# Optimization experiments

Hardware: AMD Instinct MI355X
Metric: run time of the kernel (lower is better)

Reference implementation:

```python
import jax, jax.numpy as jnp
import numpy as np

ROUTINGS = 3
NUM_CAPSULE = 32
DIM_CAPSULE = 64


def squash(x, axis=-1):
    # scale = sqrt(||x||^2 + eps) / (0.5 + ||x||^2 + eps)
    sq = jnp.sum(x * x, axis=axis, keepdims=True) + 1e-7
    return (jnp.sqrt(sq) / (0.5 + sq)) * x


def setup_inputs() -> dict:
    key = jax.random.key(0)
    k1, k2 = jax.random.split(key)
    B, IN, ID = 64, 1024, 256
    u_vecs = jax.random.normal(k1, (B, IN, ID), dtype=jnp.float32)
    # nn.Linear weight [NC*DC, ID], xavier_normal init
    fan_out, fan_in = NUM_CAPSULE * DIM_CAPSULE, ID
    std = np.sqrt(2.0 / (fan_in + fan_out)).astype(np.float32)
    W = jax.random.normal(k2, (fan_out, fan_in), dtype=jnp.float32) * std
    return {"u_vecs": u_vecs, "W": W}


def reference(u_vecs, W):
    B, IN, ID = u_vecs.shape
    # Linear projection: [B, IN, NC*DC]
    u_hat = jnp.einsum('bid,od->bio', u_vecs, W)
    # -> [B, NC, IN, DC]
    u_hat = u_hat.reshape(B, IN, NUM_CAPSULE, DIM_CAPSULE).transpose(0, 2, 1, 3)

    b = jnp.zeros((B, NUM_CAPSULE, IN), dtype=u_hat.dtype)
    o = None
    for i in range(ROUTINGS):
        c = jax.nn.softmax(b, axis=1)                      # softmax over output capsules
        o = jnp.einsum('bni,bnid->bnd', c, u_hat)          # [B, NC, DC]
        if i < ROUTINGS - 1:
            # F.normalize(o, 2, -1): x / max(||x||, 1e-12)
            norm = jnp.linalg.norm(o, axis=-1, keepdims=True)
            o = o / jnp.maximum(norm, 1e-12)
            b = jnp.einsum('bnid,bnd->bni', u_hat, o)
    return squash(o)
```

## Files before the change

kernel.cpp:

```cpp
#include <hip/hip_runtime.h>
#include <math.h>


#define B   64
#define IN  1024
#define ID  256
#define NC  32
#define DC  64

__global__ __launch_bounds__(256) void k_sumu(const float* __restrict__ u,
                                              float* __restrict__ sp0) {
    const int c = blockIdx.x, b = blockIdx.y;
    const int d = threadIdx.x;
    const float* up = u + ((size_t)b * IN + (size_t)c * (IN / 8)) * ID + d;
    float acc = 0.f;
#pragma unroll 8
    for (int i = 0; i < IN / 8; ++i) acc += up[(size_t)i * ID];
    sp0[(c * B + b) * ID + d] = acc;
}

__global__ __launch_bounds__(256) void k_ot(const float* __restrict__ W,
                                            const float* __restrict__ src,
                                            float* __restrict__ tout,
                                            const int mode) {
    const int bn = blockIdx.x;
    const int b = bn / NC, n = bn % NC;
    __shared__ float s_lds[ID];
    __shared__ float o_lds[DC];
    __shared__ float on_lds[DC];
    const int tid = threadIdx.x;

    float sv = 0.f;
    if (mode == 0) {
#pragma unroll
        for (int c = 0; c < 8; ++c) sv += src[(c * B + b) * ID + tid];
        sv *= (1.0f / NC);
    } else {
#pragma unroll
        for (int c = 0; c < 8; ++c) sv += src[((size_t)(c * B + b) * NC + n) * ID + tid];
    }
    s_lds[tid] = sv;
    __syncthreads();

    const int wave = tid >> 6, lane = tid & 63;
    const float* Wn = W + (size_t)n * DC * ID;
#pragma unroll 4
    for (int r = 0; r < 16; ++r) {
        const int d = wave * 16 + r;
        const float* wrow = Wn + (size_t)d * ID;
        float p = wrow[lane]        * s_lds[lane]
                + wrow[lane + 64]   * s_lds[lane + 64]
                + wrow[lane + 128]  * s_lds[lane + 128]
                + wrow[lane + 192]  * s_lds[lane + 192];
#pragma unroll
        for (int off = 32; off > 0; off >>= 1) p += __shfl_down(p, off);
        if (lane == 0) o_lds[d] = p;
    }
    __syncthreads();

    if (mode == 2) {
        if (tid < DC) {
            float v = o_lds[tid];
            float sq = v * v;
#pragma unroll
            for (int off = 32; off > 0; off >>= 1) sq += __shfl_down(sq, off);
            sq = __shfl(sq, 0) + 1e-7f;
            const float sc = sqrtf(sq) / (0.5f + sq);
            tout[(size_t)(b * NC + n) * DC + tid] = v * sc;
        }
        return;
    }

    if (tid < DC) {
        float v = o_lds[tid];
        float sq = v * v;
#pragma unroll
        for (int off = 32; off > 0; off >>= 1) sq += __shfl_down(sq, off);
        sq = __shfl(sq, 0);
        const float inv = 1.0f / fmaxf(sqrtf(sq), 1e-12f);
        on_lds[tid] = v * inv;
    }
    __syncthreads();

    float acc = 0.f;
    const float* wc = Wn + tid;
#pragma unroll 8
    for (int d = 0; d < DC; ++d) acc += wc[(size_t)d * ID] * on_lds[d];
    tout[((size_t)b * NC + n) * ID + tid] = acc;
}

#define ITILE 128
__global__ __launch_bounds__(256) void k_bl(const float* __restrict__ u,
                                            const float* __restrict__ t,
                                            float* __restrict__ bl) {
    const int it = blockIdx.x, b = blockIdx.y;
    const int iBase = it * ITILE;
    __shared__ float Ts[ID][36];
    __shared__ float Us[16][132];
    const int tid = threadIdx.x;

    {
        const float* tb = t + (size_t)b * NC * ID;
#pragma unroll
        for (int n = 0; n < NC; ++n) Ts[tid][n] = tb[(size_t)n * ID + tid];
    }

    const int q = tid >> 3;
    const int r = tid & 7;
    float acc[4][4] = {{0.f}};
    const float* ub = u + ((size_t)b * IN + iBase) * ID;

    for (int kc = 0; kc < ID / 16; ++kc) {
        __syncthreads();
#pragma unroll
        for (int rep = 0; rep < 2; ++rep) {
            const int f = tid + rep * 256;
            const int i = f >> 2, c4 = f & 3;
            const float4 v = *(const float4*)(ub + (size_t)i * ID + kc * 16 + c4 * 4);
            Us[c4 * 4 + 0][i] = v.x;
            Us[c4 * 4 + 1][i] = v.y;
            Us[c4 * 4 + 2][i] = v.z;
            Us[c4 * 4 + 3][i] = v.w;
        }
        __syncthreads();
#pragma unroll
        for (int k = 0; k < 16; ++k) {
            const float4 a4 = *(const float4*)&Us[k][q * 4];
            const float4 b4 = *(const float4*)&Ts[kc * 16 + k][r * 4];
            const float av[4] = {a4.x, a4.y, a4.z, a4.w};
            const float bv[4] = {b4.x, b4.y, b4.z, b4.w};
#pragma unroll
            for (int ii = 0; ii < 4; ++ii)
#pragma unroll
                for (int jj = 0; jj < 4; ++jj) acc[ii][jj] += av[ii] * bv[jj];
        }
    }

    float* blb = bl + ((size_t)b * IN + iBase) * NC;
#pragma unroll
    for (int ii = 0; ii < 4; ++ii) {
        const float4 v = make_float4(acc[ii][0], acc[ii][1], acc[ii][2], acc[ii][3]);
        *(float4*)&blb[(size_t)(q * 4 + ii) * NC + r * 4] = v;
    }
}

#define AITILE 128
__global__ __launch_bounds__(256) void k_agg(const float* __restrict__ u,
                                             const float* __restrict__ bl,
                                             float* __restrict__ sp) {
    const int c = blockIdx.x, b = blockIdx.y;
    const int iBase = c * AITILE;
    __shared__ float c_lds[AITILE][36];
    const int tid = threadIdx.x;

    {
        const int i = tid >> 1, half = tid & 1;
        const float* blp = bl + ((size_t)b * IN + iBase + i) * NC + half * 16;
        float v[16];
#pragma unroll
        for (int j = 0; j < 16; ++j) v[j] = blp[j];
        float mx = v[0];
#pragma unroll
        for (int j = 1; j < 16; ++j) mx = fmaxf(mx, v[j]);
        mx = fmaxf(mx, __shfl_xor(mx, 1));
        float sum = 0.f;
#pragma unroll
        for (int j = 0; j < 16; ++j) { v[j] = __expf(v[j] - mx); sum += v[j]; }
        sum += __shfl_xor(sum, 1);
        const float inv = 1.0f / sum;
#pragma unroll
        for (int j = 0; j < 16; ++j) c_lds[i][half * 16 + j] = v[j] * inv;
    }
    __syncthreads();

    const int d4 = tid & 63;
    const int ng = tid >> 6;
    float acc[8][4] = {{0.f}};
    const float* ub = u + ((size_t)b * IN + iBase) * ID + d4 * 4;
    for (int i = 0; i < AITILE; ++i) {
        const float4 uv = *(const float4*)(ub + (size_t)i * ID);
        const float4 c0 = *(const float4*)&c_lds[i][ng * 8];
        const float4 c1 = *(const float4*)&c_lds[i][ng * 8 + 4];
        const float cv[8] = {c0.x, c0.y, c0.z, c0.w, c1.x, c1.y, c1.z, c1.w};
        const float uvv[4] = {uv.x, uv.y, uv.z, uv.w};
#pragma unroll
        for (int j = 0; j < 8; ++j)
#pragma unroll
            for (int x = 0; x < 4; ++x) acc[j][x] += cv[j] * uvv[x];
    }

    float* spb = sp + (size_t)(c * B + b) * NC * ID;
#pragma unroll
    for (int j = 0; j < 8; ++j) {
        const int n = ng * 8 + j;
        *(float4*)&spb[(size_t)n * ID + d4 * 4] =
            make_float4(acc[j][0], acc[j][1], acc[j][2], acc[j][3]);
    }
}

extern "C" void kernel_launch(void* const* d_in, const int* in_sizes, int n_in,
                              void* d_out, int out_size, void* d_ws, size_t ws_size,
                              hipStream_t stream) {
    const float* u = (const float*)d_in[0];
    const float* W = (const float*)d_in[1];
    float* out = (float*)d_out;

    float* ws  = (float*)d_ws;
    float* t   = ws;
    float* bl  = t  + (size_t)B * NC * ID;
    float* sp  = bl + (size_t)B * IN * NC;
    float* sp0 = sp + (size_t)8 * B * NC * ID;

    const dim3 blk(256);

    k_sumu<<<dim3(8, B), blk, 0, stream>>>(u, sp0);
    k_ot  <<<dim3(B * NC), blk, 0, stream>>>(W, sp0, t, 0);
    k_bl  <<<dim3(IN / ITILE, B), blk, 0, stream>>>(u, t, bl);
    k_agg <<<dim3(IN / AITILE, B), blk, 0, stream>>>(u, bl, sp);
    k_ot  <<<dim3(B * NC), blk, 0, stream>>>(W, sp, t, 1);
    k_bl  <<<dim3(IN / ITILE, B), blk, 0, stream>>>(u, t, bl);
    k_agg <<<dim3(IN / AITILE, B), blk, 0, stream>>>(u, bl, sp);
    k_ot  <<<dim3(B * NC), blk, 0, stream>>>(W, sp, out, 2);
}
```

Measured before the change: 231.9 us.

## Fuse logits and aggregation into one routing kernel, cache W slice in LDS

```diff
diff --git a/kernel.cpp b/kernel.cpp
--- a/kernel.cpp
+++ b/kernel.cpp
@@ -7,15 +7,17 @@
 #define ID  256
 #define NC  32
 #define DC  64
+#define CH  8
+#define RIT (IN / CH)
 
 __global__ __launch_bounds__(256) void k_sumu(const float* __restrict__ u,
                                               float* __restrict__ sp0) {
     const int c = blockIdx.x, b = blockIdx.y;
     const int d = threadIdx.x;
-    const float* up = u + ((size_t)b * IN + (size_t)c * (IN / 8)) * ID + d;
+    const float* up = u + ((size_t)b * IN + (size_t)c * RIT) * ID + d;
     float acc = 0.f;
 #pragma unroll 8
-    for (int i = 0; i < IN / 8; ++i) acc += up[(size_t)i * ID];
+    for (int i = 0; i < RIT; ++i) acc += up[(size_t)i * ID];
     sp0[(c * B + b) * ID + d] = acc;
 }
 
@@ -23,79 +25,89 @@
                                             const float* __restrict__ src,
                                             float* __restrict__ tout,
                                             const int mode) {
-    const int bn = blockIdx.x;
-    const int b = bn / NC, n = bn % NC;
+    const int n = blockIdx.x, b0 = blockIdx.y * 8;
+    __shared__ float Ws[DC * ID];
     __shared__ float s_lds[ID];
     __shared__ float o_lds[DC];
     __shared__ float on_lds[DC];
     const int tid = threadIdx.x;
-
-    float sv = 0.f;
-    if (mode == 0) {
-#pragma unroll
-        for (int c = 0; c < 8; ++c) sv += src[(c * B + b) * ID + tid];
-        sv *= (1.0f / NC);
-    } else {
-#pragma unroll
-        for (int c = 0; c < 8; ++c) sv += src[((size_t)(c * B + b) * NC + n) * ID + tid];
-    }
-    s_lds[tid] = sv;
-    __syncthreads();
-
     const int wave = tid >> 6, lane = tid & 63;
-    const float* Wn = W + (size_t)n * DC * ID;
+
+    {
+        const float4* Wn4 = (const float4*)(W + (size_t)n * DC * ID);
+        float4* Ws4 = (float4*)Ws;
+#pragma unroll
+        for (int j = 0; j < (DC * ID / 4) / 256; ++j)
+            Ws4[tid + j * 256] = Wn4[tid + j * 256];
+    }
+
+    for (int bb = 0; bb < 8; ++bb) {
+        const int b = b0 + bb;
+        float sv = 0.f;
+        if (mode == 0) {
+#pragma unroll
+            for (int c = 0; c < CH; ++c) sv += src[(c * B + b) * ID + tid];
+            sv *= (1.0f / NC);
+        } else {
+#pragma unroll
+            for (int c = 0; c < CH; ++c)
+                sv += src[((size_t)(c * B + b) * NC + n) * ID + tid];
+        }
+        s_lds[tid] = sv;
+        __syncthreads();
+
 #pragma unroll 4
-    for (int r = 0; r < 16; ++r) {
-        const int d = wave * 16 + r;
-        const float* wrow = Wn + (size_t)d * ID;
-        float p = wrow[lane]        * s_lds[lane]
-                + wrow[lane + 64]   * s_lds[lane + 64]
-                + wrow[lane + 128]  * s_lds[lane + 128]
-                + wrow[lane + 192]  * s_lds[lane + 192];
-#pragma unroll
-        for (int off = 32; off > 0; off >>= 1) p += __shfl_down(p, off);
-        if (lane == 0) o_lds[d] = p;
-    }
-    __syncthreads();
-
-    if (mode == 2) {
+        for (int rr = 0; rr < 16; ++rr) {
+            const int d = wave * 16 + rr;
+            const float* wrow = Ws + d * ID;
+            float p = wrow[lane]       * s_lds[lane]
+                    + wrow[lane + 64]  * s_lds[lane + 64]
+                    + wrow[lane + 128] * s_lds[lane + 128]
+                    + wrow[lane + 192] * s_lds[lane + 192];
+#pragma unroll
+            for (int off = 32; off > 0; off >>= 1) p += __shfl_down(p, off);
+            if (lane == 0) o_lds[d] = p;
+        }
+        __syncthreads();
+
+        if (mode == 2) {
+            if (tid < DC) {
+                float v = o_lds[tid];
+                float sq = v * v;
+#pragma unroll
+                for (int off = 32; off > 0; off >>= 1) sq += __shfl_down(sq, off);
+                sq = __shfl(sq, 0) + 1e-7f;
+                const float sc = sqrtf(sq) / (0.5f + sq);
+                tout[(size_t)(b * NC + n) * DC + tid] = v * sc;
+            }
+            continue;
+        }
+
         if (tid < DC) {
             float v = o_lds[tid];
             float sq = v * v;
 #pragma unroll
             for (int off = 32; off > 0; off >>= 1) sq += __shfl_down(sq, off);
-            sq = __shfl(sq, 0) + 1e-7f;
-            const float sc = sqrtf(sq) / (0.5f + sq);
-            tout[(size_t)(b * NC + n) * DC + tid] = v * sc;
-        }
-        return;
-    }
-
-    if (tid < DC) {
-        float v = o_lds[tid];
-        float sq = v * v;
-#pragma unroll
-        for (int off = 32; off > 0; off >>= 1) sq += __shfl_down(sq, off);
-        sq = __shfl(sq, 0);
-        const float inv = 1.0f / fmaxf(sqrtf(sq), 1e-12f);
-        on_lds[tid] = v * inv;
-    }
-    __syncthreads();
-
-    float acc = 0.f;
-    const float* wc = Wn + tid;
-#pragma unroll 8
-    for (int d = 0; d < DC; ++d) acc += wc[(size_t)d * ID] * on_lds[d];
-    tout[((size_t)b * NC + n) * ID + tid] = acc;
-}
-
-#define ITILE 128
-__global__ __launch_bounds__(256) void k_bl(const float* __restrict__ u,
-                                            const float* __restrict__ t,
-                                            float* __restrict__ bl) {
-    const int it = blockIdx.x, b = blockIdx.y;
-    const int iBase = it * ITILE;
+            sq = __shfl(sq, 0);
+            on_lds[tid] = v / fmaxf(sqrtf(sq), 1e-12f);
+        }
+        __syncthreads();
+
+        float acc = 0.f;
+        const float* wc = Ws + tid;
+#pragma unroll
+        for (int d = 0; d < DC; ++d) acc += wc[d * ID] * on_lds[d];
+        tout[((size_t)b * NC + n) * ID + tid] = acc;
+    }
+}
+
+__global__ __launch_bounds__(256) void k_route(const float* __restrict__ u,
+                                               const float* __restrict__ t,
+                                               float* __restrict__ sp) {
+    const int c = blockIdx.x, b = blockIdx.y;
+    const int iBase = c * RIT;
     __shared__ float Ts[ID][36];
+    __shared__ float cl[RIT][36];
     __shared__ float Us[16][132];
     const int tid = threadIdx.x;
 
@@ -105,11 +117,9 @@
         for (int n = 0; n < NC; ++n) Ts[tid][n] = tb[(size_t)n * ID + tid];
     }
 
-    const int q = tid >> 3;
-    const int r = tid & 7;
-    float acc[4][4] = {{0.f}};
+    const int q = tid >> 3, r = tid & 7;
     const float* ub = u + ((size_t)b * IN + iBase) * ID;
-
+    float acc4[4][4] = {{0.f}};
     for (int kc = 0; kc < ID / 16; ++kc) {
         __syncthreads();
 #pragma unroll
@@ -132,33 +142,21 @@
 #pragma unroll
             for (int ii = 0; ii < 4; ++ii)
 #pragma unroll
-                for (int jj = 0; jj < 4; ++jj) acc[ii][jj] += av[ii] * bv[jj];
-        }
-    }
-
-    float* blb = bl + ((size_t)b * IN + iBase) * NC;
-#pragma unroll
-    for (int ii = 0; ii < 4; ++ii) {
-        const float4 v = make_float4(acc[ii][0], acc[ii][1], acc[ii][2], acc[ii][3]);
-        *(float4*)&blb[(size_t)(q * 4 + ii) * NC + r * 4] = v;
-    }
-}
-
-#define AITILE 128
-__global__ __launch_bounds__(256) void k_agg(const float* __restrict__ u,
-                                             const float* __restrict__ bl,
-                                             float* __restrict__ sp) {
-    const int c = blockIdx.x, b = blockIdx.y;
-    const int iBase = c * AITILE;
-    __shared__ float c_lds[AITILE][36];
-    const int tid = threadIdx.x;
+                for (int jj = 0; jj < 4; ++jj) acc4[ii][jj] += av[ii] * bv[jj];
+        }
+    }
+#pragma unroll
+    for (int ii = 0; ii < 4; ++ii)
+#pragma unroll
+        for (int jj = 0; jj < 4; ++jj)
+            cl[q * 4 + ii][r * 4 + jj] = acc4[ii][jj];
+    __syncthreads();
 
     {
         const int i = tid >> 1, half = tid & 1;
-        const float* blp = bl + ((size_t)b * IN + iBase + i) * NC + half * 16;
         float v[16];
 #pragma unroll
-        for (int j = 0; j < 16; ++j) v[j] = blp[j];
+        for (int j = 0; j < 16; ++j) v[j] = cl[i][half * 16 + j];
         float mx = v[0];
 #pragma unroll
         for (int j = 1; j < 16; ++j) mx = fmaxf(mx, v[j]);
@@ -169,18 +167,19 @@
         sum += __shfl_xor(sum, 1);
         const float inv = 1.0f / sum;
 #pragma unroll
-        for (int j = 0; j < 16; ++j) c_lds[i][half * 16 + j] = v[j] * inv;
+        for (int j = 0; j < 16; ++j) cl[i][half * 16 + j] = v[j] * inv;
     }
     __syncthreads();
 
     const int d4 = tid & 63;
     const int ng = tid >> 6;
     float acc[8][4] = {{0.f}};
-    const float* ub = u + ((size_t)b * IN + iBase) * ID + d4 * 4;
-    for (int i = 0; i < AITILE; ++i) {
-        const float4 uv = *(const float4*)(ub + (size_t)i * ID);
-        const float4 c0 = *(const float4*)&c_lds[i][ng * 8];
-        const float4 c1 = *(const float4*)&c_lds[i][ng * 8 + 4];
+    const float* up = ub + d4 * 4;
+#pragma unroll 4
+    for (int i = 0; i < RIT; ++i) {
+        const float4 uv = *(const float4*)(up + (size_t)i * ID);
+        const float4 c0 = *(const float4*)&cl[i][ng * 8];
+        const float4 c1 = *(const float4*)&cl[i][ng * 8 + 4];
         const float cv[8] = {c0.x, c0.y, c0.z, c0.w, c1.x, c1.y, c1.z, c1.w};
         const float uvv[4] = {uv.x, uv.y, uv.z, uv.w};
 #pragma unroll
@@ -188,14 +187,11 @@
 #pragma unroll
             for (int x = 0; x < 4; ++x) acc[j][x] += cv[j] * uvv[x];
     }
-
     float* spb = sp + (size_t)(c * B + b) * NC * ID;
 #pragma unroll
-    for (int j = 0; j < 8; ++j) {
-        const int n = ng * 8 + j;
-        *(float4*)&spb[(size_t)n * ID + d4 * 4] =
+    for (int j = 0; j < 8; ++j)
+        *(float4*)&spb[(size_t)(ng * 8 + j) * ID + d4 * 4] =
             make_float4(acc[j][0], acc[j][1], acc[j][2], acc[j][3]);
-    }
 }
 
 extern "C" void kernel_launch(void* const* d_in, const int* in_sizes, int n_in,
@@ -207,18 +203,15 @@
 
     float* ws  = (float*)d_ws;
     float* t   = ws;
-    float* bl  = t  + (size_t)B * NC * ID;
-    float* sp  = bl + (size_t)B * IN * NC;
-    float* sp0 = sp + (size_t)8 * B * NC * ID;
+    float* sp  = t  + (size_t)B * NC * ID;
+    float* sp0 = sp + (size_t)CH * B * NC * ID;
 
     const dim3 blk(256);
 
-    k_sumu<<<dim3(8, B), blk, 0, stream>>>(u, sp0);
-    k_ot  <<<dim3(B * NC), blk, 0, stream>>>(W, sp0, t, 0);
-    k_bl  <<<dim3(IN / ITILE, B), blk, 0, stream>>>(u, t, bl);
-    k_agg <<<dim3(IN / AITILE, B), blk, 0, stream>>>(u, bl, sp);
-    k_ot  <<<dim3(B * NC), blk, 0, stream>>>(W, sp, t, 1);
-    k_bl  <<<dim3(IN / ITILE, B), blk, 0, stream>>>(u, t, bl);
-    k_agg <<<dim3(IN / AITILE, B), blk, 0, stream>>>(u, bl, sp);
-    k_ot  <<<dim3(B * NC), blk, 0, stream>>>(W, sp, out, 2);
-}
+    k_sumu <<<dim3(CH, B),      blk, 0, stream>>>(u, sp0);
+    k_ot   <<<dim3(NC, B / 8),  blk, 0, stream>>>(W, sp0, t, 0);
+    k_route<<<dim3(CH, B),      blk, 0, stream>>>(u, t, sp);
+    k_ot   <<<dim3(NC, B / 8),  blk, 0, stream>>>(W, sp, t, 1);
+    k_route<<<dim3(CH, B),      blk, 0, stream>>>(u, t, sp);
+    k_ot   <<<dim3(NC, B / 8),  blk, 0, stream>>>(W, sp, out, 2);
+}
```

After: 301.9 us. 30.2% more time.
